# Kernel tuning notes

Hardware: AMD Instinct MI355X
Metric: run time of the kernel (lower is better)

The kernel has to match this reference:

```python
import jax, jax.numpy as jnp
import numpy as np

N = 144      # Lx*Ly lattice sites (12x12)
NH = 256     # GRU hidden units
K = 2        # local Hilbert dim (occupied/empty)
LOG_EPS = 1e-10


def _gru_step(h, x, kernel, rec_kernel, bias):
    # Keras GRU cell, reset_after=True, gate order (z, r, h)
    gx = x @ kernel + bias[0]        # [B, 3*NH]
    gh = h @ rec_kernel + bias[1]    # [B, 3*NH]
    xz, xr, xh = jnp.split(gx, 3, axis=-1)
    hz, hr, hn = jnp.split(gh, 3, axis=-1)
    z = jax.nn.sigmoid(xz + hz)
    r = jax.nn.sigmoid(xr + hr)
    hh = jnp.tanh(xh + r * hn)
    return z * h + (1.0 - z) * hh


def setup_inputs() -> dict:
    key = jax.random.key(0)
    k1, k2, k3 = jax.random.split(key, 3)
    glorot = lambda k, shape: jax.random.uniform(
        k, shape, jnp.float32,
        -jnp.sqrt(6.0 / (shape[0] + shape[1])),
        jnp.sqrt(6.0 / (shape[0] + shape[1])))
    return {
        "kernel": glorot(k1, (K, 3 * NH)),
        "rec_kernel": glorot(k2, (NH, 3 * NH)),
        "bias": jnp.zeros((2, 3 * NH), jnp.float32),
        "dense_w": glorot(k3, (NH, K)),
        "dense_b": jnp.zeros((K,), jnp.float32),
        "nsamples": 1024,
    }


def reference(kernel, rec_kernel, bias, dense_w, dense_b, nsamples):
    h0 = jnp.zeros((nsamples, NH), jnp.float32)
    x0 = jnp.zeros((nsamples, K), jnp.float32)   # 0.0 * one_hot(0)
    logP0 = jnp.zeros((nsamples,), jnp.float32)
    keys = jax.random.split(jax.random.key(42), N)

    def step(carry, step_key):
        h, x, logP = carry
        h = _gru_step(h, x, kernel, rec_kernel, bias)
        probs = jax.nn.softmax(h @ dense_w + dense_b)          # [B, K]
        log_probs = jnp.log(LOG_EPS + probs)                   # matches tf.math.log(1e-10+p)
        s = jax.random.categorical(step_key, log_probs)        # [B] int
        x_new = jax.nn.one_hot(s, K, dtype=jnp.float32)
        logP = logP + jnp.take_along_axis(log_probs, s[:, None], axis=1)[:, 0]
        return (h, x_new, logP), s

    (_, _, logP), samples = jax.lax.scan(step, (h0, x0, logP0), keys)
    samples = samples.T  # [nsamples, N]
    return samples, logP
```

## Files before the change

kernel.cpp:

```cpp
#include <hip/hip_runtime.h>
#include <stdint.h>

#define N_SITES 144
#define NHID    256
#define NSAMP   1024
#define MB      4
#define TPB     768
#define PARTITIONABLE 1

__device__ __forceinline__ uint32_t rotl32(uint32_t v, uint32_t r) {
    return (v << r) | (v >> (32u - r));
}

__device__ __forceinline__ void threefry(uint32_t k0, uint32_t k1,
                                         uint32_t x0, uint32_t x1,
                                         uint32_t& o0, uint32_t& o1) {
    uint32_t ks0 = k0, ks1 = k1, ks2 = k0 ^ k1 ^ 0x1BD11BDAu;
    x0 += ks0; x1 += ks1;
#define RG4(a,b,c,d) \
    x0 += x1; x1 = rotl32(x1,a); x1 ^= x0; \
    x0 += x1; x1 = rotl32(x1,b); x1 ^= x0; \
    x0 += x1; x1 = rotl32(x1,c); x1 ^= x0; \
    x0 += x1; x1 = rotl32(x1,d); x1 ^= x0;
    RG4(13,15,26,6)  x0 += ks1; x1 += ks2 + 1u;
    RG4(17,29,16,24) x0 += ks2; x1 += ks0 + 2u;
    RG4(13,15,26,6)  x0 += ks0; x1 += ks1 + 3u;
    RG4(17,29,16,24) x0 += ks1; x1 += ks2 + 4u;
    RG4(13,15,26,6)  x0 += ks2; x1 += ks0 + 5u;
#undef RG4
    o0 = x0; o1 = x1;
}

__device__ __forceinline__ float gumbel_from_bits(uint32_t bits) {
#pragma clang fp contract(off)
    const float TINY = 1.17549435e-38f;
    uint32_t fb = (bits >> 9) | 0x3f800000u;
    float u = __uint_as_float(fb) - 1.0f;
    u = u * (1.0f - TINY) + TINY;
    u = fmaxf(TINY, u);
    return -logf(-logf(u));
}

__global__ __launch_bounds__(TPB, 1)
void rnn_sample_kernel(const float* __restrict__ kern,
                       const float* __restrict__ rec,
                       const float* __restrict__ bias,
                       const float* __restrict__ dw,
                       const float* __restrict__ db,
                       float* __restrict__ out)
{
    const int t    = threadIdx.x;
    const int blk  = blockIdx.x;
    const int b0   = blk * MB;
    const int lane = t & 63;
    const int u    = t & 255;
    const int m1   = t >> 8;

    __shared__ float4   hs4[NHID];
    __shared__ float    pacc[MB][TPB];
    __shared__ uint32_t keyA[N_SITES], keyB[N_SITES];
    __shared__ float    glds[N_SITES][MB][2];
    __shared__ float    wred[MB][4][2];
    __shared__ int      sPrev[MB];

    const float kz0 = kern[u];        const float kr0 = kern[u + 256];  const float kn0 = kern[u + 512];
    const float kz1 = kern[768 + u];  const float kr1 = kern[768 + u + 256]; const float kn1 = kern[768 + u + 512];
    const float b0z = bias[u];        const float b0r = bias[u + 256];  const float b0n = bias[u + 512];
    const float b1z = bias[768 + u];  const float b1r = bias[768 + u + 256]; const float b1n = bias[768 + u + 512];
    const float dwa = dw[2 * u];      const float dwb = dw[2 * u + 1];
    const float dba = db[0];          const float dbb = db[1];
    float lgPr = 0.f;
    if (t < NHID) hs4[t] = make_float4(0.f, 0.f, 0.f, 0.f);
    if (t < MB) sPrev[t] = -1;
    if (t < N_SITES) {
        uint32_t o0, o1;
        threefry(0u, 42u, 0u, (uint32_t)t, o0, o1);
        keyA[t] = o0; keyB[t] = o1;
    }
    __syncthreads();

    if (t < N_SITES * MB) {
        const int n = t >> 2, m = t & 3;
        uint32_t o0a, o1a, o0b, o1b;
        const uint32_t fbase = 2u * (uint32_t)(b0 + m);
        threefry(keyA[n], keyB[n], 0u, fbase,      o0a, o1a);
        threefry(keyA[n], keyB[n], 0u, fbase + 1u, o0b, o1b);
        glds[n][m][0] = gumbel_from_bits(o0a ^ o1a);
        glds[n][m][1] = gumbel_from_bits(o0b ^ o1b);
    }
    __syncthreads();

    for (int n = 0; n < N_SITES; ++n) {
        float a0 = 0.f, a1 = 0.f, a2 = 0.f, a3 = 0.f;
        {
            const float* rp = rec + t;
#pragma unroll 8
            for (int k = 0; k < NHID; ++k) {
                float4 h4 = hs4[k];
                float w  = rp[0];
                rp += TPB;
                a0 = fmaf(h4.x, w, a0);
                a1 = fmaf(h4.y, w, a1);
                a2 = fmaf(h4.z, w, a2);
                a3 = fmaf(h4.w, w, a3);
            }
        }
        pacc[0][t] = a0; pacc[1][t] = a1; pacc[2][t] = a2; pacc[3][t] = a3;
        __syncthreads();

#pragma unroll
        for (int pass = 0; pass < 2; ++pass) {
            const int m = (pass == 0) ? m1 : 3;
            if (pass == 1 && t >= NHID) break;
            float hnew;
            {
#pragma clang fp contract(off)
                const int sp = sPrev[m];
                float xz = (sp == 0) ? kz0 : ((sp == 1) ? kz1 : 0.f);
                float xr = (sp == 0) ? kr0 : ((sp == 1) ? kr1 : 0.f);
                float xh = (sp == 0) ? kn0 : ((sp == 1) ? kn1 : 0.f);
                xz = xz + b0z;  xr = xr + b0r;  xh = xh + b0n;
                const float hz = pacc[m][u]       + b1z;
                const float hr = pacc[m][u + 256] + b1r;
                const float hn = pacc[m][u + 512] + b1n;
                const float z = 1.0f / (1.0f + expf(-(xz + hz)));
                const float r = 1.0f / (1.0f + expf(-(xr + hr)));
                const float rhn = r * hn;
                const float hh = tanhf(xh + rhn);
                const float hold = ((const float*)&hs4[u])[m];
                hnew = z * hold + (1.0f - z) * hh;
                ((float*)&hs4[u])[m] = hnew;
            }
            float va = hnew * dwa;
            float vb = hnew * dwb;
#pragma unroll
            for (int off = 32; off > 0; off >>= 1) {
                va += __shfl_xor(va, off, 64);
                vb += __shfl_xor(vb, off, 64);
            }
            if (lane == 0) { wred[m][u >> 6][0] = va; wred[m][u >> 6][1] = vb; }
        }
        __syncthreads();

        if (t < MB) {
            const int m = t;
            float l0 = wred[m][0][0] + wred[m][1][0] + wred[m][2][0] + wred[m][3][0];
            float l1 = wred[m][0][1] + wred[m][1][1] + wred[m][2][1] + wred[m][3][1];
            const float g0 = glds[n][m][0];
            const float g1 = glds[n][m][1];
            {
#pragma clang fp contract(off)
                l0 = l0 + dba;
                l1 = l1 + dbb;
                const float mx = fmaxf(l0, l1);
                const float e0 = expf(l0 - mx), e1 = expf(l1 - mx);
                const float den = e0 + e1;
                const float lp0 = logf(1e-10f + e0 / den);
                const float lp1 = logf(1e-10f + e1 / den);
                const float v0 = g0 + lp0;
                const float v1 = g1 + lp1;
                const int s = (v1 > v0) ? 1 : 0;
                sPrev[m] = s;
                lgPr = lgPr + (s ? lp1 : lp0);
                out[(size_t)(b0 + m) * N_SITES + n] = (float)s;
            }
        }
    }

    if (t < MB) out[(size_t)NSAMP * N_SITES + (b0 + t)] = lgPr;
}

extern "C" void kernel_launch(void* const* d_in, const int* in_sizes, int n_in,
                              void* d_out, int out_size, void* d_ws, size_t ws_size,
                              hipStream_t stream) {
    (void)in_sizes; (void)n_in; (void)d_ws; (void)ws_size; (void)out_size;
    const float* kern = (const float*)d_in[0];
    const float* rec  = (const float*)d_in[1];
    const float* bias = (const float*)d_in[2];
    const float* dwp  = (const float*)d_in[3];
    const float* dbp  = (const float*)d_in[4];
    float* out = (float*)d_out;
    rnn_sample_kernel<<<NSAMP / MB, TPB, 0, stream>>>(kern, rec, bias, dwp, dbp, out);
}
```

Baseline: 1.472 ms.

## Split block into matvec and gate warp groups with flag-based pipelining

Warp-specializes the block: 12 warps do the recurrent matvec while 4 extra warps compute the GRU gates, logits and sampling. Per-tile flags and a double-buffered hidden state replace block-wide barriers, so matvec warps can start on each 64-row tile of h as soon as it is ready. The recurrent weights are also repacked into float4 quads in the workspace to allow 128-bit loads. The cost is spin-waiting on LDS flags, a serialized single-lane sampling step, and an extra repack launch on every call.

```diff
diff --git a/kernel.cpp b/kernel.cpp
--- a/kernel.cpp
+++ b/kernel.cpp
@@ -5,8 +5,12 @@
 #define NHID    256
 #define NSAMP   1024
 #define MB      4
-#define TPB     768
+#define TPB     1024
+#define NAW     12
 #define PARTITIONABLE 1
+
+#define LD(p)    __hip_atomic_load((p), __ATOMIC_ACQUIRE, __HIP_MEMORY_SCOPE_WORKGROUP)
+#define ST(p, v) __hip_atomic_store((p), (v), __ATOMIC_RELEASE, __HIP_MEMORY_SCOPE_WORKGROUP)
 
 __device__ __forceinline__ uint32_t rotl32(uint32_t v, uint32_t r) {
     return (v << r) | (v >> (32u - r));
@@ -41,6 +45,14 @@
     return -logf(-logf(u));
 }
 
+__global__ void repack_rec(const float* __restrict__ rec,
+                           float* __restrict__ recQ) {
+    const int col = blockIdx.x;
+    const int k   = threadIdx.x;
+    recQ[((size_t)(k >> 2) * 768 + col) * 4 + (k & 3)] = rec[(size_t)k * 768 + col];
+}
+
+template <bool QUAD>
 __global__ __launch_bounds__(TPB, 1)
 void rnn_sample_kernel(const float* __restrict__ kern,
                        const float* __restrict__ rec,
@@ -52,33 +64,32 @@
     const int t    = threadIdx.x;
     const int blk  = blockIdx.x;
     const int b0   = blk * MB;
+    const int wid  = t >> 6;
     const int lane = t & 63;
-    const int u    = t & 255;
-    const int m1   = t >> 8;
-
-    __shared__ float4   hs4[NHID];
-    __shared__ float    pacc[MB][TPB];
+
+    __shared__ float4   hbuf[2][NHID];
+    __shared__ float    pacc[MB][768];
     __shared__ uint32_t keyA[N_SITES], keyB[N_SITES];
     __shared__ float    glds[N_SITES][MB][2];
     __shared__ float    wred[MB][4][2];
     __shared__ int      sPrev[MB];
-
-    const float kz0 = kern[u];        const float kr0 = kern[u + 256];  const float kn0 = kern[u + 512];
-    const float kz1 = kern[768 + u];  const float kr1 = kern[768 + u + 256]; const float kn1 = kern[768 + u + 512];
-    const float b0z = bias[u];        const float b0r = bias[u + 256];  const float b0n = bias[u + 512];
-    const float b1z = bias[768 + u];  const float b1r = bias[768 + u + 256]; const float b1n = bias[768 + u + 512];
-    const float dwa = dw[2 * u];      const float dwb = dw[2 * u + 1];
-    const float dba = db[0];          const float dbb = db[1];
-    float lgPr = 0.f;
-    if (t < NHID) hs4[t] = make_float4(0.f, 0.f, 0.f, 0.f);
-    if (t < MB) sPrev[t] = -1;
+    __shared__ int hflag[4];
+    __shared__ int paccflag[NAW];
+    __shared__ int gdone[4];
+    __shared__ int wflag[4];
+    __shared__ int sflag;
+
+    if (t < NHID) { hbuf[0][t] = make_float4(0.f,0.f,0.f,0.f); hbuf[1][t] = make_float4(0.f,0.f,0.f,0.f); }
+    if (t < MB)  sPrev[t] = -1;
+    if (t < 4)   { hflag[t] = 1; gdone[t] = 0; wflag[t] = 0; }
+    if (t < NAW) paccflag[t] = 0;
+    if (t == 0)  sflag = 0;
     if (t < N_SITES) {
         uint32_t o0, o1;
         threefry(0u, 42u, 0u, (uint32_t)t, o0, o1);
         keyA[t] = o0; keyB[t] = o1;
     }
     __syncthreads();
-
     if (t < N_SITES * MB) {
         const int n = t >> 2, m = t & 3;
         uint32_t o0a, o1a, o0b, o1b;
@@ -90,95 +101,164 @@
     }
     __syncthreads();
 
-    for (int n = 0; n < N_SITES; ++n) {
-        float a0 = 0.f, a1 = 0.f, a2 = 0.f, a3 = 0.f;
-        {
-            const float* rp = rec + t;
+    if (wid < NAW) {
+        for (int n = 0; n < N_SITES; ++n) {
+            const float4* hb = hbuf[n & 1];
+            float a0 = 0.f, a1 = 0.f, a2 = 0.f, a3 = 0.f;
+            if (QUAD) {
+                const float4* rq = reinterpret_cast<const float4*>(rec) + t;
+                for (int T = 0; T < 4; ++T) {
+                    while (LD(&hflag[T]) < n + 1) {}
+#pragma unroll
+                    for (int g = 0; g < 16; ++g) {
+                        const int gg = 16 * T + g;
+                        const float4 w = rq[(size_t)gg * 768];
+                        float4 h4 = hb[4 * gg + 0];
+                        a0 = fmaf(h4.x, w.x, a0); a1 = fmaf(h4.y, w.x, a1);
+                        a2 = fmaf(h4.z, w.x, a2); a3 = fmaf(h4.w, w.x, a3);
+                        h4 = hb[4 * gg + 1];
+                        a0 = fmaf(h4.x, w.y, a0); a1 = fmaf(h4.y, w.y, a1);
+                        a2 = fmaf(h4.z, w.y, a2); a3 = fmaf(h4.w, w.y, a3);
+                        h4 = hb[4 * gg + 2];
+                        a0 = fmaf(h4.x, w.z, a0); a1 = fmaf(h4.y, w.z, a1);
+                        a2 = fmaf(h4.z, w.z, a2); a3 = fmaf(h4.w, w.z, a3);
+                        h4 = hb[4 * gg + 3];
+                        a0 = fmaf(h4.x, w.w, a0); a1 = fmaf(h4.y, w.w, a1);
+                        a2 = fmaf(h4.z, w.w, a2); a3 = fmaf(h4.w, w.w, a3);
+                    }
+                }
+            } else {
+                const float* rp = rec + t;
+                for (int T = 0; T < 4; ++T) {
+                    while (LD(&hflag[T]) < n + 1) {}
 #pragma unroll 8
-            for (int k = 0; k < NHID; ++k) {
-                float4 h4 = hs4[k];
-                float w  = rp[0];
-                rp += TPB;
-                a0 = fmaf(h4.x, w, a0);
-                a1 = fmaf(h4.y, w, a1);
-                a2 = fmaf(h4.z, w, a2);
-                a3 = fmaf(h4.w, w, a3);
-            }
+                    for (int k = 64 * T; k < 64 * T + 64; ++k) {
+                        float4 h4 = hb[k];
+                        float w  = rp[(size_t)k * 768];
+                        a0 = fmaf(h4.x, w, a0); a1 = fmaf(h4.y, w, a1);
+                        a2 = fmaf(h4.z, w, a2); a3 = fmaf(h4.w, w, a3);
+                    }
+                }
+            }
+            while (LD(&gdone[wid & 3]) < n) {}
+            pacc[0][t] = a0; pacc[1][t] = a1; pacc[2][t] = a2; pacc[3][t] = a3;
+            if (lane == 0) ST(&paccflag[wid], n + 1);
         }
-        pacc[0][t] = a0; pacc[1][t] = a1; pacc[2][t] = a2; pacc[3][t] = a3;
-        __syncthreads();
-
-#pragma unroll
-        for (int pass = 0; pass < 2; ++pass) {
-            const int m = (pass == 0) ? m1 : 3;
-            if (pass == 1 && t >= NHID) break;
-            float hnew;
+    } else {
+        const int g = wid - NAW;
+        const int u = (g << 6) | lane;
+        const float kz0 = kern[u];        const float kr0 = kern[u + 256];       const float kn0 = kern[u + 512];
+        const float kz1 = kern[768 + u];  const float kr1 = kern[768 + u + 256]; const float kn1 = kern[768 + u + 512];
+        const float b0z = bias[u];        const float b0r = bias[u + 256];       const float b0n = bias[u + 512];
+        const float b1z = bias[768 + u];  const float b1r = bias[768 + u + 256]; const float b1n = bias[768 + u + 512];
+        const float dwa = dw[2 * u];      const float dwb = dw[2 * u + 1];
+        const float dba = db[0];          const float dbb = db[1];
+        float lgP0 = 0.f, lgP1 = 0.f, lgP2 = 0.f, lgP3 = 0.f;
+
+        for (int n = 0; n < N_SITES; ++n) {
+            while (LD(&sflag) < n) __builtin_amdgcn_s_sleep(1);
+            const int sp0 = sPrev[0], sp1 = sPrev[1], sp2 = sPrev[2], sp3 = sPrev[3];
+            while (LD(&paccflag[g    ]) < n + 1) __builtin_amdgcn_s_sleep(1);
+            while (LD(&paccflag[g + 4]) < n + 1) __builtin_amdgcn_s_sleep(1);
+            while (LD(&paccflag[g + 8]) < n + 1) __builtin_amdgcn_s_sleep(1);
+
+            const float4 ho = hbuf[n & 1][u];
+            const float hold[MB] = { ho.x, ho.y, ho.z, ho.w };
+            const int   spA[MB]  = { sp0, sp1, sp2, sp3 };
+            float hnew[MB];
             {
 #pragma clang fp contract(off)
-                const int sp = sPrev[m];
-                float xz = (sp == 0) ? kz0 : ((sp == 1) ? kz1 : 0.f);
-                float xr = (sp == 0) ? kr0 : ((sp == 1) ? kr1 : 0.f);
-                float xh = (sp == 0) ? kn0 : ((sp == 1) ? kn1 : 0.f);
-                xz = xz + b0z;  xr = xr + b0r;  xh = xh + b0n;
-                const float hz = pacc[m][u]       + b1z;
-                const float hr = pacc[m][u + 256] + b1r;
-                const float hn = pacc[m][u + 512] + b1n;
-                const float z = 1.0f / (1.0f + expf(-(xz + hz)));
-                const float r = 1.0f / (1.0f + expf(-(xr + hr)));
-                const float rhn = r * hn;
-                const float hh = tanhf(xh + rhn);
-                const float hold = ((const float*)&hs4[u])[m];
-                hnew = z * hold + (1.0f - z) * hh;
-                ((float*)&hs4[u])[m] = hnew;
-            }
-            float va = hnew * dwa;
-            float vb = hnew * dwb;
-#pragma unroll
-            for (int off = 32; off > 0; off >>= 1) {
-                va += __shfl_xor(va, off, 64);
-                vb += __shfl_xor(vb, off, 64);
-            }
-            if (lane == 0) { wred[m][u >> 6][0] = va; wred[m][u >> 6][1] = vb; }
+#pragma unroll
+                for (int m = 0; m < MB; ++m) {
+                    const int sp = spA[m];
+                    float xz = (sp == 0) ? kz0 : ((sp == 1) ? kz1 : 0.f);
+                    float xr = (sp == 0) ? kr0 : ((sp == 1) ? kr1 : 0.f);
+                    float xh = (sp == 0) ? kn0 : ((sp == 1) ? kn1 : 0.f);
+                    xz = xz + b0z;  xr = xr + b0r;  xh = xh + b0n;
+                    const float hz = pacc[m][u]       + b1z;
+                    const float hr = pacc[m][u + 256] + b1r;
+                    const float hn = pacc[m][u + 512] + b1n;
+                    const float z = 1.0f / (1.0f + expf(-(xz + hz)));
+                    const float r = 1.0f / (1.0f + expf(-(xr + hr)));
+                    const float rhn = r * hn;
+                    const float hh = tanhf(xh + rhn);
+                    hnew[m] = z * hold[m] + (1.0f - z) * hh;
+                }
+            }
+            if (lane == 0) ST(&gdone[g], n + 1);
+            hbuf[(n + 1) & 1][u] = make_float4(hnew[0], hnew[1], hnew[2], hnew[3]);
+            if (lane == 0) ST(&hflag[g], n + 2);
+
+#pragma unroll
+            for (int m = 0; m < MB; ++m) {
+                float va = hnew[m] * dwa;
+                float vb = hnew[m] * dwb;
+#pragma unroll
+                for (int off = 32; off > 0; off >>= 1) {
+                    va += __shfl_xor(va, off, 64);
+                    vb += __shfl_xor(vb, off, 64);
+                }
+                if (lane == 0) { wred[m][g][0] = va; wred[m][g][1] = vb; }
+            }
+            if (lane == 0) ST(&wflag[g], n + 1);
+
+            if (g == 0 && lane == 0) {
+                while (LD(&wflag[0]) < n + 1) {}
+                while (LD(&wflag[1]) < n + 1) {}
+                while (LD(&wflag[2]) < n + 1) {}
+                while (LD(&wflag[3]) < n + 1) {}
+#pragma unroll
+                for (int m = 0; m < MB; ++m) {
+#pragma clang fp contract(off)
+                    const float l0r = wred[m][0][0] + wred[m][1][0] + wred[m][2][0] + wred[m][3][0];
+                    const float l1r = wred[m][0][1] + wred[m][1][1] + wred[m][2][1] + wred[m][3][1];
+                    const float g0 = glds[n][m][0];
+                    const float g1 = glds[n][m][1];
+                    const float l0 = l0r + dba;
+                    const float l1 = l1r + dbb;
+                    const float mx = fmaxf(l0, l1);
+                    const float e0 = expf(l0 - mx), e1 = expf(l1 - mx);
+                    const float den = e0 + e1;
+                    const float lp0 = logf(1e-10f + e0 / den);
+                    const float lp1 = logf(1e-10f + e1 / den);
+                    const float v0 = g0 + lp0;
+                    const float v1 = g1 + lp1;
+                    const int s = (v1 > v0) ? 1 : 0;
+                    sPrev[m] = s;
+                    const float d = s ? lp1 : lp0;
+                    if (m == 0) lgP0 += d; else if (m == 1) lgP1 += d;
+                    else if (m == 2) lgP2 += d; else lgP3 += d;
+                    out[(size_t)(b0 + m) * N_SITES + n] = (float)s;
+                }
+                ST(&sflag, n + 1);
+            }
         }
-        __syncthreads();
-
-        if (t < MB) {
-            const int m = t;
-            float l0 = wred[m][0][0] + wred[m][1][0] + wred[m][2][0] + wred[m][3][0];
-            float l1 = wred[m][0][1] + wred[m][1][1] + wred[m][2][1] + wred[m][3][1];
-            const float g0 = glds[n][m][0];
-            const float g1 = glds[n][m][1];
-            {
-#pragma clang fp contract(off)
-                l0 = l0 + dba;
-                l1 = l1 + dbb;
-                const float mx = fmaxf(l0, l1);
-                const float e0 = expf(l0 - mx), e1 = expf(l1 - mx);
-                const float den = e0 + e1;
-                const float lp0 = logf(1e-10f + e0 / den);
-                const float lp1 = logf(1e-10f + e1 / den);
-                const float v0 = g0 + lp0;
-                const float v1 = g1 + lp1;
-                const int s = (v1 > v0) ? 1 : 0;
-                sPrev[m] = s;
-                lgPr = lgPr + (s ? lp1 : lp0);
-                out[(size_t)(b0 + m) * N_SITES + n] = (float)s;
-            }
+        if (g == 0 && lane == 0) {
+            out[(size_t)NSAMP * N_SITES + b0 + 0] = lgP0;
+            out[(size_t)NSAMP * N_SITES + b0 + 1] = lgP1;
+            out[(size_t)NSAMP * N_SITES + b0 + 2] = lgP2;
+            out[(size_t)NSAMP * N_SITES + b0 + 3] = lgP3;
         }
     }
-
-    if (t < MB) out[(size_t)NSAMP * N_SITES + (b0 + t)] = lgPr;
 }
 
 extern "C" void kernel_launch(void* const* d_in, const int* in_sizes, int n_in,
                               void* d_out, int out_size, void* d_ws, size_t ws_size,
                               hipStream_t stream) {
-    (void)in_sizes; (void)n_in; (void)d_ws; (void)ws_size; (void)out_size;
+    (void)in_sizes; (void)n_in; (void)out_size;
     const float* kern = (const float*)d_in[0];
     const float* rec  = (const float*)d_in[1];
     const float* bias = (const float*)d_in[2];
     const float* dwp  = (const float*)d_in[3];
     const float* dbp  = (const float*)d_in[4];
     float* out = (float*)d_out;
-    rnn_sample_kernel<<<NSAMP / MB, TPB, 0, stream>>>(kern, rec, bias, dwp, dbp, out);
-}
+
+    const size_t needQ = sizeof(float) * (size_t)NHID * 768;
+    if (d_ws != nullptr && ws_size >= needQ) {
+        float* recQ = (float*)d_ws;
+        repack_rec<<<768, NHID, 0, stream>>>(rec, recQ);
+        rnn_sample_kernel<true><<<NSAMP / MB, TPB, 0, stream>>>(kern, recQ, bias, dwp, dbp, out);
+    } else {
+        rnn_sample_kernel<false><<<NSAMP / MB, TPB, 0, stream>>>(kern, rec, bias, dwp, dbp, out);
+    }
+}
```

Result: faster. 1.368 ms (-7.1%).
